# Kernel optimization log

Hardware: AMD Instinct MI355X
Metric: run time of the kernel (lower is better)

Reference implementation:

```python
import jax, jax.numpy as jnp
import numpy as np

B, S, D, K, NS = 4, 2048, 768, 8192, 2
TAU = 1.0


def setup_inputs() -> dict:
    key = jax.random.key(0)
    k1, k2, k3, k4 = jax.random.split(key, 4)
    x = jax.random.normal(k1, (B, S, D), dtype=jnp.float32)
    w_codebook = jax.random.normal(k2, (K, D), dtype=jnp.float32) * (1.0 / np.sqrt(D))
    embeddings = jax.random.normal(k3, (K, D), dtype=jnp.float32)
    # standard Gumbel(0,1) noise, one draw per (token, sample, code)
    gumbel_noise = jax.random.gumbel(k4, (B, S, NS, K), dtype=jnp.float32)
    return {"x": x, "w_codebook": w_codebook, "embeddings": embeddings,
            "gumbel_noise": gumbel_noise, "num_samples": NS}


def reference(x, w_codebook, embeddings, gumbel_noise, num_samples):
    # logits = Linear(x) without bias: [B, S, K]
    logits = jnp.einsum('bsd,kd->bsk', x, w_codebook)
    # expand over num_samples and add Gumbel noise (F.gumbel_softmax, training)
    g = (logits[:, :, None, :] + gumbel_noise) / TAU          # [B, S, NS, K]
    y_soft = jax.nn.softmax(g, axis=-1)
    # hard one-hot with straight-through estimator (hard=True, hard_p=1.0)
    idx = jnp.argmax(y_soft, axis=-1)                          # [B, S, NS]
    y_hard = jax.nn.one_hot(idx, K, dtype=y_soft.dtype)
    indices = y_hard + y_soft - jax.lax.stop_gradient(y_soft)  # [B, S, NS, K]
    # one-hot matmul == gather of codebook rows
    emb = jnp.einsum('bsnk,kd->bsnd', indices, embeddings)     # [B, S, NS, D]
    return emb, indices
```

## Files before the change

kernel.cpp:

```cpp
#include <hip/hip_runtime.h>
#include <stdint.h>

#define Bc 4
#define Sc 2048
#define Dc 768
#define Kc 8192
#define NSc 2
#define Mc (Bc*Sc)
#define EMB_ELEMS ((size_t)Mc*NSc*Dc)

typedef __attribute__((ext_vector_type(8))) __bf16 bf16x8;
typedef __attribute__((ext_vector_type(4))) float f32x4;
typedef __attribute__((ext_vector_type(4))) unsigned short u16x4;
typedef __attribute__((ext_vector_type(8))) unsigned short u16x8;

__device__ __forceinline__ unsigned short f2bf(float f){
  unsigned int u = __float_as_uint(f);
  u += 0x7FFFu + ((u >> 16) & 1u);
  return (unsigned short)(u >> 16);
}
__device__ __forceinline__ float bf2f(unsigned short h){
  return __uint_as_float(((unsigned int)h) << 16);
}

__global__ __launch_bounds__(256) void k_convert(const float4* __restrict__ x,
                                                 const float4* __restrict__ w,
                                                 u16x4* __restrict__ xb,
                                                 u16x4* __restrict__ wb){
  int i = blockIdx.x * 256 + threadIdx.x;
  float4 v = x[i];
  u16x4 o;
  o.x = f2bf(v.x); o.y = f2bf(v.y); o.z = f2bf(v.z); o.w = f2bf(v.w);
  xb[i] = o;
  v = w[i];
  o.x = f2bf(v.x); o.y = f2bf(v.y); o.z = f2bf(v.z); o.w = f2bf(v.w);
  wb[i] = o;
}

#define BM 128
#define BN 128
#define BK 32

__global__ __launch_bounds__(512, 2) void k_gemm(const unsigned short* __restrict__ xb,
                                                 const unsigned short* __restrict__ wb,
                                                 unsigned short* stash){
  __shared__ __align__(16) unsigned char lds[131072];

  const int tid  = threadIdx.x;
  const int lane = tid & 63;
  const int wid  = tid >> 6;
  const int wr   = wid >> 2;
  const int wc   = wid & 3;
  const int fr   = lane & 15;
  const int fq   = lane >> 4;

  const int bid = (int)blockIdx.x;
  const int xcd = bid & 7;
  const int ii  = bid >> 3;
  const int bm0 = (ii >> 2) * 256;
  const int bn0 = (xcd * 4 + (ii & 3)) * 256;

  float* zbase = (float*)stash;
  const int zpan = bn0 >> 8;

  f32x4 acc[8][4] = {};

  const int rin   = tid >> 3;
  const int kblkp = (tid & 7) ^ (rin & 7);
  const unsigned short* gsrc[8];
  unsigned dstoff[8];
  #pragma unroll
  for (int s = 0; s < 8; ++s) {
    const int isA = s >> 2;
    const int q   = s & 3;
    const int r64 = isA ? (((q & 1) << 1) | (q >> 1)) : q;
    const int grow = (isA ? bm0 : bn0) + r64 * 64 + rin;
    gsrc[s]   = (isA ? xb : wb) + (size_t)grow * Dc + kblkp * 8;
    dstoff[s] = (isA ? 0u : 32768u) + (unsigned)r64 * 8192u + (unsigned)wid * 1024u;
  }

#define ISSUE(s_, bo_) __builtin_amdgcn_global_load_lds( \
    (const __attribute__((address_space(1))) void*)gsrc[s_], \
    (__attribute__((address_space(3))) void*)&lds[(bo_) + dstoff[s_]], 16, 0, 0)

#define ZSTORE(u_) do { \
    const unsigned g_ = (unsigned)(t*4 + (u_))*512u + (unsigned)tid; \
    const unsigned tl_ = g_ / 96u, j4_ = g_ - tl_*96u; \
    const f32x4 z_ = {0.f, 0.f, 0.f, 0.f}; \
    __builtin_nontemporal_store(z_, (f32x4*)(zbase + \
        (size_t)(bm0 + tl_)*16384 + 4096 + zpan*384 + j4_*4)); \
  } while (0)

  #pragma unroll
  for (int s = 0; s < 8; ++s) ISSUE(s, 0u);
  #pragma unroll
  for (int s = 0; s < 8; ++s) gsrc[s] += 64;

  unsigned bufR = 0u, bufW = 65536u;
  const unsigned aRow = (unsigned)(wr*128 + fr) * 128u;
  const unsigned bRow = (unsigned)(wc*64  + fr) * 128u + 32768u;
  const unsigned sl0  = (unsigned)((fq       ) ^ (fr & 7)) * 16u;
  const unsigned sl1  = (unsigned)((fq + 4   ) ^ (fr & 7)) * 16u;

  for (int t = 0; t < 12; ++t) {
    const bool more = (t < 11);
    bf16x8 a[4], b0[4], b1[4];

    if (t == 0) asm volatile("s_waitcnt vmcnt(2)" ::: "memory");
    else        asm volatile("s_waitcnt vmcnt(6)" ::: "memory");
    __builtin_amdgcn_s_barrier();
    asm volatile("" ::: "memory");
    if (more) { ISSUE(0, bufW); ISSUE(1, bufW); }
    #pragma unroll
    for (int n = 0; n < 4; ++n) b0[n] = *(const bf16x8*)&lds[bufR + bRow + (unsigned)n*2048u + sl0];
    #pragma unroll
    for (int m = 0; m < 4; ++m) a[m]  = *(const bf16x8*)&lds[bufR + aRow + (unsigned)m*2048u + sl0];
    __builtin_amdgcn_s_setprio(1);
    #pragma unroll
    for (int m = 0; m < 4; ++m)
      #pragma unroll
      for (int n = 0; n < 4; ++n)
        acc[m][n] = __builtin_amdgcn_mfma_f32_16x16x32_bf16(a[m], b0[n], acc[m][n], 0, 0, 0);
    __builtin_amdgcn_s_setprio(0);

    if (!more)      asm volatile("s_waitcnt vmcnt(0)" ::: "memory");
    else if (t == 0) asm volatile("s_waitcnt vmcnt(2)" ::: "memory");
    else            asm volatile("s_waitcnt vmcnt(4)" ::: "memory");
    __builtin_amdgcn_s_barrier();
    asm volatile("" ::: "memory");
    if (more) { ISSUE(2, bufW); ISSUE(3, bufW); }
    #pragma unroll
    for (int m = 0; m < 4; ++m) a[m] = *(const bf16x8*)&lds[bufR + aRow + 8192u + (unsigned)m*2048u + sl0];
    __builtin_amdgcn_s_setprio(1);
    #pragma unroll
    for (int m = 0; m < 4; ++m)
      #pragma unroll
      for (int n = 0; n < 4; ++n)
        acc[4+m][n] = __builtin_amdgcn_mfma_f32_16x16x32_bf16(a[m], b0[n], acc[4+m][n], 0, 0, 0);
    __builtin_amdgcn_s_setprio(0);

    if (more) { ISSUE(4, bufW); ISSUE(5, bufW); }
    asm volatile("" ::: "memory");
    ZSTORE(0); ZSTORE(1);
    asm volatile("" ::: "memory");
    #pragma unroll
    for (int n = 0; n < 4; ++n) b1[n] = *(const bf16x8*)&lds[bufR + bRow + (unsigned)n*2048u + sl1];
    #pragma unroll
    for (int m = 0; m < 4; ++m) a[m]  = *(const bf16x8*)&lds[bufR + aRow + (unsigned)m*2048u + sl1];
    __builtin_amdgcn_s_setprio(1);
    #pragma unroll
    for (int m = 0; m < 4; ++m)
      #pragma unroll
      for (int n = 0; n < 4; ++n)
        acc[m][n] = __builtin_amdgcn_mfma_f32_16x16x32_bf16(a[m], b1[n], acc[m][n], 0, 0, 0);
    __builtin_amdgcn_s_setprio(0);

    if (more) { ISSUE(6, bufW); ISSUE(7, bufW); }
    asm volatile("" ::: "memory");
    ZSTORE(2); ZSTORE(3);
    asm volatile("" ::: "memory");
    #pragma unroll
    for (int m = 0; m < 4; ++m) a[m] = *(const bf16x8*)&lds[bufR + aRow + 8192u + (unsigned)m*2048u + sl1];
    __builtin_amdgcn_s_setprio(1);
    #pragma unroll
    for (int m = 0; m < 4; ++m)
      #pragma unroll
      for (int n = 0; n < 4; ++n)
        acc[4+m][n] = __builtin_amdgcn_mfma_f32_16x16x32_bf16(a[m], b1[n], acc[4+m][n], 0, 0, 0);
    __builtin_amdgcn_s_setprio(0);

    bufR ^= 65536u; bufW ^= 65536u;
    if (t < 10) {
      #pragma unroll
      for (int s = 0; s < 8; ++s) gsrc[s] += 64;
    }
  }
#undef ZSTORE
#undef ISSUE

  unsigned short* tb16 = (unsigned short*)lds;
  #pragma unroll
  for (int h = 0; h < 2; ++h) {
    __syncthreads();
    if (wr == h) {
      #pragma unroll
      for (int m = 0; m < 8; ++m)
        #pragma unroll
        for (int n = 0; n < 4; ++n)
          #pragma unroll
          for (int r = 0; r < 4; ++r)
            tb16[(m*16 + fq*4 + r)*264 + (wc*64 + n*16 + fr)] = f2bf(acc[m][n][r]);
    }
    __syncthreads();
    #pragma unroll
    for (int i = 0; i < 8; ++i) {
      const int n = i*512 + tid;
      const int row = n >> 5, seg = n & 31;
      *(u16x8*)&stash[(size_t)(bm0 + h*128 + row) * 32768 + bn0 + seg*8] =
          *(const u16x8*)&tb16[row*264 + seg*8];
    }
  }
}

#define MARGIN 0.125f

__global__ __launch_bounds__(256) void k_select(const unsigned short* logits,
                                                const float* __restrict__ gumbel,
                                                const float* __restrict__ x,
                                                const float* __restrict__ w,
                                                const float* __restrict__ emb_tab,
                                                float* __restrict__ out_emb,
                                                float* out_ind){
  const int t   = blockIdx.x;
  const int tid = threadIdx.x;
  const int lane = tid & 63, wid = tid >> 6;

  __shared__ unsigned short Lrow[Kc];
  __shared__ float wmax[4];
  __shared__ int   cand_k[16];
  __shared__ float cand_g[16];
  __shared__ int   cand_cnt;
  __shared__ int   sel_idx[NSc];

  {
    const u16x4* src = (const u16x4*)(logits + (size_t)t * 32768);
    u16x4* dst = (u16x4*)Lrow;
    #pragma unroll
    for (int j = 0; j < 8; j++) dst[j*256 + tid] = src[j*256 + tid];
  }
  __syncthreads();

  for (int s = 0; s < NSc; ++s) {
    const float* grow = gumbel + ((size_t)t * NSc + s) * Kc;
    float4 vals[8];
    float m = -1e30f;
    #pragma unroll
    for (int j = 0; j < 8; j++) {
      float4 g4 = ((const float4*)grow)[j*256 + tid];
      u16x4 l4 = *(const u16x4*)&Lrow[j*1024 + tid*4];
      float4 v;
      v.x = bf2f(l4.x) + g4.x;
      v.y = bf2f(l4.y) + g4.y;
      v.z = bf2f(l4.z) + g4.z;
      v.w = bf2f(l4.w) + g4.w;
      vals[j] = v;
      m = fmaxf(m, fmaxf(fmaxf(v.x, v.y), fmaxf(v.z, v.w)));
    }
    #pragma unroll
    for (int off = 32; off; off >>= 1) m = fmaxf(m, __shfl_xor(m, off));
    if (lane == 0) wmax[wid] = m;
    __syncthreads();
    const float gmax = fmaxf(fmaxf(wmax[0], wmax[1]), fmaxf(wmax[2], wmax[3]));
    if (tid == 0) cand_cnt = 0;
    __syncthreads();

    const float thr = gmax - MARGIN;
    #pragma unroll
    for (int j = 0; j < 8; j++) {
      const int k0 = j*1024 + tid*4;
      float vv[4] = {vals[j].x, vals[j].y, vals[j].z, vals[j].w};
      #pragma unroll
      for (int q = 0; q < 4; q++) {
        if (vv[q] >= thr) {
          int p = atomicAdd(&cand_cnt, 1);
          if (p < 16) cand_k[p] = k0 + q;
        }
      }
    }
    __syncthreads();

    const int cnt = min(cand_cnt, 16);
    if (cnt == 1) {
      if (tid == 0) sel_idx[s] = cand_k[0];
    } else {
      for (int c = wid; c < cnt; c += 4) {
        const int kc = cand_k[c];
        const float* wr = w + (size_t)kc * Dc;
        const float* xr = x + (size_t)t * Dc;
        double accd = 0.0;
        for (int d = lane; d < Dc; d += 64) accd += (double)xr[d] * (double)wr[d];
        #pragma unroll
        for (int off = 32; off; off >>= 1) accd += __shfl_xor(accd, off);
        if (lane == 0) cand_g[c] = (float)accd + grow[kc];
      }
      __syncthreads();
      if (tid == 0) {
        float bg = -1e30f; int bk_ = Kc;
        for (int c = 0; c < cnt; c++) {
          float g = cand_g[c]; int kk = cand_k[c];
          if (g > bg || (g == bg && kk < bk_)) { bg = g; bk_ = kk; }
        }
        sel_idx[s] = bk_;
      }
    }
    __syncthreads();
  }

  {
    float* row0lo = out_ind + (size_t)t * 16384;
    const float4 z = {0.f, 0.f, 0.f, 0.f};
    #pragma unroll
    for (int q = 0; q < 4; ++q)
      ((float4*)row0lo)[q*256 + tid] = z;
  }
  __syncthreads();
  if (tid == 0) {
    out_ind[(size_t)t*16384 +        sel_idx[0]] = 1.0f;
    out_ind[(size_t)t*16384 + 8192 + sel_idx[1]] = 1.0f;
  }

  #pragma unroll
  for (int s = 0; s < NSc; ++s) {
    const float* er = emb_tab + (size_t)sel_idx[s] * Dc;
    float* eo = out_emb + ((size_t)t*NSc + s)*Dc;
    for (int d = tid; d < Dc; d += 256) eo[d] = er[d];
  }
}

extern "C" void kernel_launch(void* const* d_in, const int* in_sizes, int n_in,
                              void* d_out, int out_size, void* d_ws, size_t ws_size,
                              hipStream_t stream) {
  const float* x   = (const float*)d_in[0];
  const float* w   = (const float*)d_in[1];
  const float* emb = (const float*)d_in[2];
  const float* gum = (const float*)d_in[3];

  float* out_emb = (float*)d_out;
  float* out_ind = out_emb + EMB_ELEMS;
  unsigned short* stash = (unsigned short*)out_ind;

  unsigned short* xb = (unsigned short*)d_ws;
  unsigned short* wb = xb + (size_t)Mc * Dc;

  const int n4 = (Mc * Dc) / 4;
  k_convert<<<n4 / 256, 256, 0, stream>>>((const float4*)x, (const float4*)w,
                                          (u16x4*)xb, (u16x4*)wb);
  k_gemm<<<1024, 512, 0, stream>>>(xb, wb, stash);
  k_select<<<Mc, 256, 0, stream>>>(stash, gum, x, w, emb, out_emb, out_ind);
}
```

Before: 332.2 us.

## Prune argmax search with per-slice logit maxima computed in GEMM epilogue

The GEMM epilogue now writes a bf16 maximum of the logits for each 64-wide code slice per token into a stats buffer that reuses the embedding output region. The select kernel combines these slice maxima with per-slice Gumbel maxima to get upper bounds, then reads only the logit slices that can still hold the winner, instead of copying the full 8192-entry logit row into LDS. This cuts logit reads from the stash at the cost of extra shuffles in the GEMM epilogue, more barriers in select, and relying on a bound margin that rounding could break.

```diff
diff --git a/kernel.cpp b/kernel.cpp
--- a/kernel.cpp
+++ b/kernel.cpp
@@ -43,7 +43,8 @@
 
 __global__ __launch_bounds__(512, 2) void k_gemm(const unsigned short* __restrict__ xb,
                                                  const unsigned short* __restrict__ wb,
-                                                 unsigned short* stash){
+                                                 unsigned short* stash,
+                                                 unsigned short* statsb){
   __shared__ __align__(16) unsigned char lds[131072];
 
   const int tid  = threadIdx.x;
@@ -123,9 +124,9 @@
         acc[m][n] = __builtin_amdgcn_mfma_f32_16x16x32_bf16(a[m], b0[n], acc[m][n], 0, 0, 0);
     __builtin_amdgcn_s_setprio(0);
 
-    if (!more)      asm volatile("s_waitcnt vmcnt(0)" ::: "memory");
+    if (!more)       asm volatile("s_waitcnt vmcnt(0)" ::: "memory");
     else if (t == 0) asm volatile("s_waitcnt vmcnt(2)" ::: "memory");
-    else            asm volatile("s_waitcnt vmcnt(4)" ::: "memory");
+    else             asm volatile("s_waitcnt vmcnt(4)" ::: "memory");
     __builtin_amdgcn_s_barrier();
     asm volatile("" ::: "memory");
     if (more) { ISSUE(2, bufW); ISSUE(3, bufW); }
@@ -177,6 +178,23 @@
   }
 #undef ZSTORE
 #undef ISSUE
+
+  #pragma unroll
+  for (int m = 0; m < 8; ++m)
+    #pragma unroll
+    for (int r = 0; r < 4; ++r) {
+      float mx = fmaxf(fmaxf(acc[m][0][r], acc[m][1][r]),
+                       fmaxf(acc[m][2][r], acc[m][3][r]));
+      mx = fmaxf(mx, __shfl_xor(mx, 1));
+      mx = fmaxf(mx, __shfl_xor(mx, 2));
+      mx = fmaxf(mx, __shfl_xor(mx, 4));
+      mx = fmaxf(mx, __shfl_xor(mx, 8));
+      if (fr == 0) {
+        const int tok = bm0 + wr*128 + m*16 + fq*4 + r;
+        __builtin_nontemporal_store(f2bf(mx),
+            &statsb[(size_t)tok * 3072 + (bn0 >> 6) + wc]);
+      }
+    }
 
   unsigned short* tb16 = (unsigned short*)lds;
   #pragma unroll
@@ -204,67 +222,103 @@
 
 #define MARGIN 0.125f
 
-__global__ __launch_bounds__(256) void k_select(const unsigned short* logits,
+__global__ __launch_bounds__(256) void k_select(const unsigned short* stash,
+                                                const unsigned short* statsb,
                                                 const float* __restrict__ gumbel,
                                                 const float* __restrict__ x,
                                                 const float* __restrict__ w,
                                                 const float* __restrict__ emb_tab,
-                                                float* __restrict__ out_emb,
+                                                float* out_emb,
                                                 float* out_ind){
   const int t   = blockIdx.x;
   const int tid = threadIdx.x;
   const int lane = tid & 63, wid = tid >> 6;
 
-  __shared__ unsigned short Lrow[Kc];
-  __shared__ float wmax[4];
+  __shared__ float gm[128];
+  __shared__ unsigned short sml[128];
+  __shared__ float wred[4];
+  __shared__ int   wredi[4];
+  __shared__ int   bslice;
+  __shared__ float lbv;
+  __shared__ int   Vint;
+  __shared__ int   slist[128];
+  __shared__ int   scnt;
   __shared__ int   cand_k[16];
   __shared__ float cand_g[16];
   __shared__ int   cand_cnt;
   __shared__ int   sel_idx[NSc];
 
-  {
-    const u16x4* src = (const u16x4*)(logits + (size_t)t * 32768);
-    u16x4* dst = (u16x4*)Lrow;
-    #pragma unroll
-    for (int j = 0; j < 8; j++) dst[j*256 + tid] = src[j*256 + tid];
-  }
+  if (tid < 64)
+    ((unsigned int*)sml)[tid] = ((const unsigned int*)(statsb + (size_t)t*3072))[tid];
+  const unsigned short* srow = stash + (size_t)t * 32768;
   __syncthreads();
 
   for (int s = 0; s < NSc; ++s) {
     const float* grow = gumbel + ((size_t)t * NSc + s) * Kc;
-    float4 vals[8];
-    float m = -1e30f;
-    #pragma unroll
-    for (int j = 0; j < 8; j++) {
-      float4 g4 = ((const float4*)grow)[j*256 + tid];
-      u16x4 l4 = *(const u16x4*)&Lrow[j*1024 + tid*4];
-      float4 v;
-      v.x = bf2f(l4.x) + g4.x;
-      v.y = bf2f(l4.y) + g4.y;
-      v.z = bf2f(l4.z) + g4.z;
-      v.w = bf2f(l4.w) + g4.w;
-      vals[j] = v;
-      m = fmaxf(m, fmaxf(fmaxf(v.x, v.y), fmaxf(v.z, v.w)));
-    }
-    #pragma unroll
-    for (int off = 32; off; off >>= 1) m = fmaxf(m, __shfl_xor(m, off));
-    if (lane == 0) wmax[wid] = m;
-    __syncthreads();
-    const float gmax = fmaxf(fmaxf(wmax[0], wmax[1]), fmaxf(wmax[2], wmax[3]));
-    if (tid == 0) cand_cnt = 0;
-    __syncthreads();
-
-    const float thr = gmax - MARGIN;
-    #pragma unroll
-    for (int j = 0; j < 8; j++) {
-      const int k0 = j*1024 + tid*4;
-      float vv[4] = {vals[j].x, vals[j].y, vals[j].z, vals[j].w};
-      #pragma unroll
-      for (int q = 0; q < 4; q++) {
-        if (vv[q] >= thr) {
-          int p = atomicAdd(&cand_cnt, 1);
-          if (p < 16) cand_k[p] = k0 + q;
-        }
+    if (tid == 0) { scnt = 0; cand_cnt = 0; }
+
+    #pragma unroll
+    for (int j = 0; j < 8; ++j) {
+      const float4 g4 = ((const float4*)grow)[j*256 + tid];
+      float m4 = fmaxf(fmaxf(g4.x, g4.y), fmaxf(g4.z, g4.w));
+      m4 = fmaxf(m4, __shfl_xor(m4, 1));
+      m4 = fmaxf(m4, __shfl_xor(m4, 2));
+      m4 = fmaxf(m4, __shfl_xor(m4, 4));
+      m4 = fmaxf(m4, __shfl_xor(m4, 8));
+      if ((tid & 15) == 0) gm[j*16 + (tid >> 4)] = m4;
+    }
+    __syncthreads();
+
+    float ub = -1e30f; int si = 0;
+    if (tid < 128) { ub = gm[tid] + bf2f(sml[tid]); si = tid; }
+    #pragma unroll
+    for (int off = 1; off < 64; off <<= 1) {
+      const float ov = __shfl_xor(ub, off); const int oi = __shfl_xor(si, off);
+      if (ov > ub || (ov == ub && oi < si)) { ub = ov; si = oi; }
+    }
+    if (lane == 0) { wred[wid] = ub; wredi[wid] = si; }
+    __syncthreads();
+    if (tid == 0) {
+      float b = wred[0]; int bi = wredi[0];
+      #pragma unroll
+      for (int q = 1; q < 4; ++q)
+        if (wred[q] > b || (wred[q] == b && wredi[q] < bi)) { b = wred[q]; bi = wredi[q]; }
+      bslice = bi;
+    }
+    __syncthreads();
+
+    if (wid == 0) {
+      const int k = bslice*64 + lane;
+      float v = bf2f(srow[k]) + grow[k];
+      #pragma unroll
+      for (int off = 1; off < 64; off <<= 1) v = fmaxf(v, __shfl_xor(v, off));
+      if (lane == 0) { lbv = v; Vint = __float_as_int(v); }
+    }
+    __syncthreads();
+
+    if (tid < 128) {
+      if (gm[tid] + bf2f(sml[tid]) >= lbv - MARGIN - 0.05f)
+        slist[atomicAdd(&scnt, 1)] = tid;
+    }
+    __syncthreads();
+    const int sc = scnt;
+
+    for (int i = wid; i < sc; i += 4) {
+      const int k = slist[i]*64 + lane;
+      float v = bf2f(srow[k]) + grow[k];
+      #pragma unroll
+      for (int off = 1; off < 64; off <<= 1) v = fmaxf(v, __shfl_xor(v, off));
+      if (lane == 0) atomicMax(&Vint, __float_as_int(v));
+    }
+    __syncthreads();
+    const float V = __int_as_float(Vint);
+
+    for (int i = wid; i < sc; i += 4) {
+      const int k = slist[i]*64 + lane;
+      const float v = bf2f(srow[k]) + grow[k];
+      if (v >= V - MARGIN) {
+        const int p = atomicAdd(&cand_cnt, 1);
+        if (p < 16) cand_k[p] = k;
       }
     }
     __syncthreads();
@@ -285,12 +339,12 @@
       }
       __syncthreads();
       if (tid == 0) {
-        float bg = -1e30f; int bk_ = Kc;
-        for (int c = 0; c < cnt; c++) {
-          float g = cand_g[c]; int kk = cand_k[c];
-          if (g > bg || (g == bg && kk < bk_)) { bg = g; bk_ = kk; }
+        float bg = -1e30f; int bk = Kc;
+        for (int c = 0; c < cnt; ++c) {
+          const float gg = cand_g[c]; const int kk = cand_k[c];
+          if (gg > bg || (gg == bg && kk < bk)) { bg = gg; bk = kk; }
         }
-        sel_idx[s] = bk_;
+        sel_idx[s] = bk;
       }
     }
     __syncthreads();
@@ -327,7 +381,8 @@
 
   float* out_emb = (float*)d_out;
   float* out_ind = out_emb + EMB_ELEMS;
-  unsigned short* stash = (unsigned short*)out_ind;
+  unsigned short* stash  = (unsigned short*)out_ind;
+  unsigned short* statsb = (unsigned short*)out_emb;
 
   unsigned short* xb = (unsigned short*)d_ws;
   unsigned short* wb = xb + (size_t)Mc * Dc;
@@ -335,6 +390,6 @@
   const int n4 = (Mc * Dc) / 4;
   k_convert<<<n4 / 256, 256, 0, stream>>>((const float4*)x, (const float4*)w,
                                           (u16x4*)xb, (u16x4*)wb);
-  k_gemm<<<1024, 512, 0, stream>>>(xb, wb, stash);
-  k_select<<<Mc, 256, 0, stream>>>(stash, gum, x, w, emb, out_emb, out_ind);
-}
+  k_gemm<<<1024, 512, 0, stream>>>(xb, wb, stash, statsb);
+  k_select<<<Mc, 256, 0, stream>>>(stash, statsb, gum, x, w, emb, out_emb, out_ind);
+}
```

Measured after the change: 390.9 us. 1.18x slower.
